# Optimization experiments

Measured on AMD Instinct MI355X. Metric: run time of the kernel, lower is better.

## Reference

```python
import jax, jax.numpy as jnp
import numpy as np

B, N, DIN, D, E, STEP = 4, 1024, 256, 256, 5, 5


def setup_inputs() -> dict:
    key = jax.random.key(0)
    ks = jax.random.split(key, 14)
    s = 0.02  # weight init scale
    inp = {
        "node_features": jax.random.normal(ks[0], (B, N, DIN), dtype=jnp.float32),
        # dense per-edge-type adjacency; scaled so messages stay in a sane range
        "adj_matrices": jax.random.uniform(ks[1], (B, E, N, N), dtype=jnp.float32) * (2.0 / N),
        "fc_in_w": jax.random.normal(ks[2], (D, DIN), dtype=jnp.float32) * s,
        "fc_in_b": jnp.zeros((D,), dtype=jnp.float32),
        "edge_w": jax.random.normal(ks[3], (E, D, D), dtype=jnp.float32) * s,
        "edge_b": jax.random.normal(ks[4], (E, D), dtype=jnp.float32) * s,
        "gru_w_ih": jax.random.normal(ks[5], (3 * D, D), dtype=jnp.float32) * s,
        "gru_w_hh": jax.random.normal(ks[6], (3 * D, D), dtype=jnp.float32) * s,
        "gru_b_ih": jnp.zeros((3 * D,), dtype=jnp.float32),
        "gru_b_hh": jnp.zeros((3 * D,), dtype=jnp.float32),
        "conv1_w": jax.random.normal(ks[7], (D, D), dtype=jnp.float32) * s,
        "conv1_b": jnp.zeros((D,), dtype=jnp.float32),
        "conv2_w": jax.random.normal(ks[8], (D, D), dtype=jnp.float32) * s,
        "conv2_b": jnp.zeros((D,), dtype=jnp.float32),
    }
    return inp


def _gru_cell(x, h, w_ih, w_hh, b_ih, b_hh):
    # torch GRUCell: gates ordered [r, z, n]
    gi = x @ w_ih.T + b_ih  # [B*N, 3D]
    gh = h @ w_hh.T + b_hh
    ir, iz, inn = jnp.split(gi, 3, axis=-1)
    hr, hz, hn = jnp.split(gh, 3, axis=-1)
    r = jax.nn.sigmoid(ir + hr)
    z = jax.nn.sigmoid(iz + hz)
    n = jnp.tanh(inn + r * hn)
    return (1.0 - z) * n + z * h


def reference(node_features, adj_matrices, fc_in_w, fc_in_b, edge_w, edge_b,
              gru_w_ih, gru_w_hh, gru_b_ih, gru_b_hh,
              conv1_w, conv1_b, conv2_w, conv2_b):
    h = node_features @ fc_in_w.T + fc_in_b  # [B, N, D]
    sum_edge_b = jnp.sum(edge_b, axis=0)  # accumulated biases over edge types
    for _ in range(STEP):
        # messages per edge type: adj_e @ h  -> [B, E, N, D]
        msgs = jnp.einsum('benm,bmd->bend', adj_matrices, h)
        # per-edge-type linear (y = x @ W_e.T) then accumulate over edge types
        acc = jnp.einsum('bend,ekd->bnk', msgs, edge_w) + sum_edge_b  # [B, N, D]
        h = _gru_cell(acc, h, gru_w_ih, gru_w_hh, gru_b_ih, gru_b_hh)
    node_states = h  # [B, N, D]
    # conv1d with kernel_size=1 over node axis == per-node linear on channels
    attn_weights = jax.nn.sigmoid(node_states @ conv1_w.T + conv1_b)  # [B, N, D]
    feats = jnp.tanh(node_states @ conv2_w.T + conv2_b)  # [B, N, D]
    graph_embedding = jnp.sum(attn_weights * feats, axis=1)  # sum over nodes -> [B, D]
    attn_map = jnp.mean(attn_weights, axis=2)  # mean over channels -> [B, N]
    return (graph_embedding, node_states, attn_map)
```

## Files before the change

### kernel.cpp

```cpp
#include <hip/hip_runtime.h>
#include <hip/hip_bf16.h>
#include <cstdint>


typedef __attribute__((ext_vector_type(8))) short bf16x8;
typedef __attribute__((ext_vector_type(4))) float f32x4;

__device__ __forceinline__ float bf2f(__hip_bfloat16 x) { return __bfloat162float(x); }
__device__ __forceinline__ __hip_bfloat16 f2bf(float x) { return __float2bfloat16(x); }
__device__ __forceinline__ short f2bs(float x) {
  __hip_bfloat16 h = __float2bfloat16(x);
  return *reinterpret_cast<short*>(&h);
}
__device__ __forceinline__ float s2f(short x) {
  __hip_bfloat16 h = *reinterpret_cast<__hip_bfloat16*>(&x);
  return __bfloat162float(h);
}

__device__ __forceinline__ bf16x8 ld8_ext(const void* base, long off, bool f32) {
  if (f32) {
    const float* p = (const float*)base + off;
    bf16x8 r;
#pragma unroll
    for (int i = 0; i < 8; ++i) r[i] = f2bs(p[i]);
    return r;
  }
  return *(const bf16x8*)((const __hip_bfloat16*)base + off);
}

__device__ __forceinline__ bf16x8 ld8_sum5(const __hip_bfloat16* part, int row, int k) {
  const long base = (long)row * 256 + (long)(row >> 10) * 1048576 + k;
  float s[8] = {0.f, 0.f, 0.f, 0.f, 0.f, 0.f, 0.f, 0.f};
#pragma unroll
  for (int e = 0; e < 5; ++e) {
    bf16x8 v = *(const bf16x8*)(part + base + e * 262144);
#pragma unroll
    for (int j = 0; j < 8; ++j) s[j] += s2f(v[j]);
  }
  bf16x8 r;
#pragma unroll
  for (int j = 0; j < 8; ++j) r[j] = f2bs(s[j]);
  return r;
}

__global__ void detect_dtype(const uint32_t* __restrict__ raw, int* __restrict__ flag) {
  __shared__ int cnt;
  if (threadIdx.x == 0) cnt = 0;
  __syncthreads();
  int c = 0;
  for (int i = threadIdx.x; i < 512; i += 256) {
    uint32_t byte = (raw[i] >> 8) & 0xFF;
    if (byte >= 0x28 && byte <= 0x40) ++c;
  }
  atomicAdd(&cnt, c);
  __syncthreads();
  if (threadIdx.x == 0) *flag = (cnt < 300) ? 1 : 0;
}

__global__ void prep_pool(const void* fcb, const void* bih, const void* bhh,
                          const void* c1b, const void* c2b, const void* edgeb,
                          const int* __restrict__ flag,
                          float* __restrict__ pool, float* __restrict__ ge,
                          float* __restrict__ am32) {
  const bool f32 = (*flag != 0);
  for (int t = threadIdx.x; t < 2560; t += 256) {
    const void* p; int i;
    if (t < 256)       { p = fcb;  i = t; }
    else if (t < 1024) { p = bih;  i = t - 256; }
    else if (t < 1792) { p = bhh;  i = t - 1024; }
    else if (t < 2048) { p = c1b;  i = t - 1792; }
    else if (t < 2304) { p = c2b;  i = t - 2048; }
    else {
      int k = t - 2304; float s = 0.f;
      for (int e = 0; e < 5; ++e)
        s += f32 ? ((const float*)edgeb)[e * 256 + k]
                 : bf2f(((const __hip_bfloat16*)edgeb)[e * 256 + k]);
      pool[t] = s; continue;
    }
    pool[t] = f32 ? ((const float*)p)[i] : bf2f(((const __hip_bfloat16*)p)[i]);
  }
  for (int t = threadIdx.x; t < 1024; t += 256) ge[t] = 0.f;
  for (int t = threadIdx.x; t < 4096; t += 256) am32[t] = 0.f;
}

__global__ void bias_gi_k(const float* __restrict__ pool,
                          const __hip_bfloat16* __restrict__ wih,
                          float* __restrict__ out) {
  const int n = blockIdx.x * 256 + threadIdx.x;
  if (n >= 768) return;
  float s = pool[256 + n];
  for (int k = 0; k < 256; ++k) s += pool[2304 + k] * bf2f(wih[n * 256 + k]);
  out[n] = s;
}

__global__ void wcvt_all(const void* fcw, const void* edw, const void* wih,
                         const void* whh, const void* c1w, const void* c2w,
                         const int* __restrict__ flag, __hip_bfloat16* __restrict__ dst) {
  const bool f32 = (*flag != 0);
  const int i = blockIdx.x * 256 + threadIdx.x;
  const void* src; int off;
  if      (i < 65536)  { src = fcw; off = i; }
  else if (i < 393216) { src = edw; off = i - 65536; }
  else if (i < 589824) { src = wih; off = i - 393216; }
  else if (i < 786432) { src = whh; off = i - 589824; }
  else if (i < 851968) { src = c1w; off = i - 786432; }
  else                 { src = c2w; off = i - 851968; }
  dst[i] = f32 ? f2bf(((const float*)src)[off])
               : ((const __hip_bfloat16*)src)[off];
}

__global__ void adj_cvt(const void* __restrict__ src, const int* __restrict__ flag,
                        __hip_bfloat16* __restrict__ dst) {
  const bool f32 = (*flag != 0);
  const long i = ((long)blockIdx.x * 256 + threadIdx.x) * 8;
  bf16x8 r;
  if (f32) {
    const float* p = (const float*)src + i;
#pragma unroll
    for (int j = 0; j < 8; ++j) r[j] = f2bs(p[j]);
  } else {
    r = *(const bf16x8*)((const __hip_bfloat16*)src + i);
  }
  *(bf16x8*)(dst + i) = r;
}

template<int OUT_MODE, bool HAS_BIAS, int A_MODE, bool DUAL>
__global__ __launch_bounds__(256)
void gemm_bt(const void* __restrict__ A, const __hip_bfloat16* __restrict__ Bt,
             const float* __restrict__ bias, void* __restrict__ Cp,
             const void* __restrict__ A2, const __hip_bfloat16* __restrict__ Bt2,
             const float* __restrict__ bias2, void* __restrict__ Cp2,
             const int* __restrict__ flag,
             int Kg, int ngrp, int lda, int ldb, int ldc,
             long aBatch, int zdivA, int zmodA,
             long bBatch, int zdivB, int zmodB,
             long cBatch, int zdivC, long aGrp, long bGrp, int zSplit)
{
  __shared__ __align__(16) __hip_bfloat16 sA[64 * 64];
  __shared__ __align__(16) __hip_bfloat16 sB[64 * 64];
  const bool af32 = (A_MODE == 1) ? (*flag != 0) : false;
  const int t = threadIdx.x;
  const int w = t >> 6;
  const int l = t & 63;
  const int m0 = blockIdx.x * 64;
  const int n0 = blockIdx.y * 64;
  int z = blockIdx.z;

  const void* Au = A; const __hip_bfloat16* Btu = Bt;
  const float* biasu = bias; void* Cpu = Cp;
  bool second = false;
  if (DUAL && z >= zSplit) {
    Au = A2; Btu = Bt2; biasu = bias2; Cpu = Cp2; z -= zSplit; second = true;
  }

  const long aOff = (long)((z / zdivA) % zmodA) * aBatch;
  const __hip_bfloat16* Bb = Btu + (long)((z / zdivB) % zmodB) * bBatch;

  const int p0 = t, p1 = t + 256;
  const int sr0 = p0 >> 3, sc0 = (p0 & 7) ^ (sr0 & 7);
  const int sr1 = p1 >> 3, sc1 = (p1 & 7) ^ (sr1 & 7);

  f32x4 acc[4];
#pragma unroll
  for (int i = 0; i < 4; ++i) acc[i] = (f32x4){0.f, 0.f, 0.f, 0.f};

  const int mrow = w * 16 + (l & 15);
  const int quad = l >> 4;

  for (int g = 0; g < ngrp; ++g) {
    const long aG = aOff + (long)g * aGrp;
    const __hip_bfloat16* Bg = Bb + (long)g * bGrp;
    for (int k0 = 0; k0 < Kg; k0 += 64) {
      bf16x8 a0, a1;
      if (A_MODE == 2 && !second) {
        a0 = ld8_sum5((const __hip_bfloat16*)Au, m0 + sr0, k0 + sc0 * 8);
        a1 = ld8_sum5((const __hip_bfloat16*)Au, m0 + sr1, k0 + sc1 * 8);
      } else if (A_MODE == 1) {
        a0 = ld8_ext(Au, aG + (long)(m0 + sr0) * lda + (k0 + sc0 * 8), af32);
        a1 = ld8_ext(Au, aG + (long)(m0 + sr1) * lda + (k0 + sc1 * 8), af32);
      } else {
        const __hip_bfloat16* Ab = (const __hip_bfloat16*)Au;
        a0 = *(const bf16x8*)(Ab + aG + (long)(m0 + sr0) * lda + (k0 + sc0 * 8));
        a1 = *(const bf16x8*)(Ab + aG + (long)(m0 + sr1) * lda + (k0 + sc1 * 8));
      }
      bf16x8 b0 = *(const bf16x8*)(Bg + (long)(n0 + sr0) * ldb + (k0 + sc0 * 8));
      bf16x8 b1 = *(const bf16x8*)(Bg + (long)(n0 + sr1) * ldb + (k0 + sc1 * 8));
      __syncthreads();
      *(bf16x8*)(sA + p0 * 8) = a0;
      *(bf16x8*)(sA + p1 * 8) = a1;
      *(bf16x8*)(sB + p0 * 8) = b0;
      *(bf16x8*)(sB + p1 * 8) = b1;
      __syncthreads();
#pragma unroll
      for (int ks = 0; ks < 2; ++ks) {
        const int cg = ks * 4 + quad;
        bf16x8 af = *(const bf16x8*)(sA + mrow * 64 + ((cg ^ (mrow & 7)) * 8));
#pragma unroll
        for (int t4 = 0; t4 < 4; ++t4) {
          const int nrow = t4 * 16 + (l & 15);
          bf16x8 bfr = *(const bf16x8*)(sB + nrow * 64 + ((cg ^ (nrow & 7)) * 8));
          acc[t4] = __builtin_amdgcn_mfma_f32_16x16x32_bf16(af, bfr, acc[t4], 0, 0, 0);
        }
      }
    }
  }

  const long cOff = (long)(z / zdivC) * cBatch;
#pragma unroll
  for (int t4 = 0; t4 < 4; ++t4) {
    const int n = n0 + t4 * 16 + (l & 15);
    float bv = 0.f;
    if (HAS_BIAS) bv = biasu[n];
#pragma unroll
    for (int r = 0; r < 4; ++r) {
      const int m = m0 + w * 16 + quad * 4 + r;
      const float v = acc[t4][r] + bv;
      if (OUT_MODE == 0)
        ((__hip_bfloat16*)Cpu)[cOff + (long)m * ldc + n] = f2bf(v);
      else
        ((float*)Cpu)[cOff + (long)m * ldc + n] = v;
    }
  }
}

__global__ void gru_gate(const __hip_bfloat16* __restrict__ gi,
                         const __hip_bfloat16* __restrict__ gh,
                         __hip_bfloat16* __restrict__ hbf,
                         void* __restrict__ ns_out, const int* __restrict__ flag)
{
  const int m = blockIdx.x;
  const int k = threadIdx.x;
  const long gb = (long)m * 768;
  const float ir = bf2f(gi[gb + k]);
  const float iz = bf2f(gi[gb + 256 + k]);
  const float inn = bf2f(gi[gb + 512 + k]);
  const float hr = bf2f(gh[gb + k]);
  const float hz = bf2f(gh[gb + 256 + k]);
  const float hn = bf2f(gh[gb + 512 + k]);
  const long hidx = (long)m * 256 + k;
  const float h = bf2f(hbf[hidx]);
  const float r = 1.f / (1.f + __expf(-(ir + hr)));
  const float zz = 1.f / (1.f + __expf(-(iz + hz)));
  const float nn = tanhf(inn + r * hn);
  const float hnew = (1.f - zz) * nn + zz * h;
  const __hip_bfloat16 hb = f2bf(hnew);
  hbf[hidx] = hb;
  if (ns_out) {
    if (*flag) ((float*)ns_out)[1024 + hidx] = hnew;
    else       ((__hip_bfloat16*)ns_out)[1024 + hidx] = hb;
  }
}

__global__ __launch_bounds__(256)
void conv_fused(const __hip_bfloat16* __restrict__ hbf,
                const __hip_bfloat16* __restrict__ c1w,
                const __hip_bfloat16* __restrict__ c2w,
                const float* __restrict__ pool,
                float* __restrict__ geg, float* __restrict__ am32)
{
  __shared__ __align__(16) __hip_bfloat16 sA[64 * 64];
  __shared__ __align__(16) __hip_bfloat16 sB1[64 * 64];
  __shared__ __align__(16) __hip_bfloat16 sB2[64 * 64];
  __shared__ float sge[64];
  __shared__ float sam[64];
  const int t = threadIdx.x, w = t >> 6, l = t & 63;
  const int m0 = blockIdx.x * 64, n0 = blockIdx.y * 64;
  if (t < 64) { sge[t] = 0.f; sam[t] = 0.f; }
  const int p0 = t, p1 = t + 256;
  const int sr0 = p0 >> 3, sc0 = (p0 & 7) ^ (sr0 & 7);
  const int sr1 = p1 >> 3, sc1 = (p1 & 7) ^ (sr1 & 7);
  f32x4 a1[4], a2[4];
#pragma unroll
  for (int i = 0; i < 4; ++i) { a1[i] = (f32x4){0,0,0,0}; a2[i] = (f32x4){0,0,0,0}; }
  const int mrow = w * 16 + (l & 15);
  const int quad = l >> 4;
  for (int k0 = 0; k0 < 256; k0 += 64) {
    bf16x8 va0 = *(const bf16x8*)(hbf + (long)(m0 + sr0) * 256 + (k0 + sc0 * 8));
    bf16x8 va1 = *(const bf16x8*)(hbf + (long)(m0 + sr1) * 256 + (k0 + sc1 * 8));
    bf16x8 vb0 = *(const bf16x8*)(c1w + (long)(n0 + sr0) * 256 + (k0 + sc0 * 8));
    bf16x8 vb1 = *(const bf16x8*)(c1w + (long)(n0 + sr1) * 256 + (k0 + sc1 * 8));
    bf16x8 vc0 = *(const bf16x8*)(c2w + (long)(n0 + sr0) * 256 + (k0 + sc0 * 8));
    bf16x8 vc1 = *(const bf16x8*)(c2w + (long)(n0 + sr1) * 256 + (k0 + sc1 * 8));
    __syncthreads();
    *(bf16x8*)(sA + p0 * 8) = va0;  *(bf16x8*)(sA + p1 * 8) = va1;
    *(bf16x8*)(sB1 + p0 * 8) = vb0; *(bf16x8*)(sB1 + p1 * 8) = vb1;
    *(bf16x8*)(sB2 + p0 * 8) = vc0; *(bf16x8*)(sB2 + p1 * 8) = vc1;
    __syncthreads();
#pragma unroll
    for (int ks = 0; ks < 2; ++ks) {
      const int cg = ks * 4 + quad;
      bf16x8 af = *(const bf16x8*)(sA + mrow * 64 + ((cg ^ (mrow & 7)) * 8));
#pragma unroll
      for (int t4 = 0; t4 < 4; ++t4) {
        const int nrow = t4 * 16 + (l & 15);
        bf16x8 b1f = *(const bf16x8*)(sB1 + nrow * 64 + ((cg ^ (nrow & 7)) * 8));
        bf16x8 b2f = *(const bf16x8*)(sB2 + nrow * 64 + ((cg ^ (nrow & 7)) * 8));
        a1[t4] = __builtin_amdgcn_mfma_f32_16x16x32_bf16(af, b1f, a1[t4], 0, 0, 0);
        a2[t4] = __builtin_amdgcn_mfma_f32_16x16x32_bf16(af, b2f, a2[t4], 0, 0, 0);
      }
    }
  }
  float asum[4] = {0.f, 0.f, 0.f, 0.f};
#pragma unroll
  for (int t4 = 0; t4 < 4; ++t4) {
    const int n = n0 + t4 * 16 + (l & 15);
    const float bb1 = pool[1792 + n], bb2 = pool[2048 + n];
    float g = 0.f;
#pragma unroll
    for (int r = 0; r < 4; ++r) {
      const float av = 1.f / (1.f + __expf(-(a1[t4][r] + bb1)));
      const float fv = tanhf(a2[t4][r] + bb2);
      g += av * fv;
      asum[r] += av;
    }
    atomicAdd(&sge[t4 * 16 + (l & 15)], g);
  }
#pragma unroll
  for (int r = 0; r < 4; ++r) atomicAdd(&sam[w * 16 + quad * 4 + r], asum[r]);
  __syncthreads();
  if (t < 64) atomicAdd(&geg[(m0 >> 10) * 256 + n0 + t], sge[t]);
  else if (t < 128) atomicAdd(&am32[m0 + (t - 64)], sam[t - 64]);
}

__global__ void finish_out(const float* __restrict__ ge, const float* __restrict__ am32,
                           void* __restrict__ dout, const int* __restrict__ flag)
{
  const int t = blockIdx.x * 256 + threadIdx.x;
  const bool f32 = (*flag != 0);
  if (t < 1024) {
    if (f32) ((float*)dout)[t] = ge[t];
    else     ((__hip_bfloat16*)dout)[t] = f2bf(ge[t]);
  } else {
    const float v = am32[t - 1024] * (1.f / 256.f);
    if (f32) ((float*)dout)[1049600 + t - 1024] = v;
    else     ((__hip_bfloat16*)dout)[1049600 + t - 1024] = f2bf(v);
  }
}

extern "C" void kernel_launch(void* const* d_in, const int* in_sizes, int n_in,
                              void* d_out, int out_size, void* d_ws, size_t ws_size,
                              hipStream_t stream) {
  (void)in_sizes; (void)n_in; (void)out_size;
  const void* node_f = d_in[0];
  const void* adj    = d_in[1];
  const void* fc_w   = d_in[2];
  const void* fc_b   = d_in[3];
  const void* edge_w = d_in[4];
  const void* edge_b = d_in[5];
  const void* w_ih   = d_in[6];
  const void* w_hh   = d_in[7];
  const void* b_ih   = d_in[8];
  const void* b_hh   = d_in[9];
  const void* c1w    = d_in[10];
  const void* c1b    = d_in[11];
  const void* c2w    = d_in[12];
  const void* c2b    = d_in[13];

  char* ws = (char*)d_ws;
  const size_t MB = (size_t)1 << 20;
  int*            flag = (int*)(ws);
  float*          bp   = (float*)(ws + 256);
  float*          ge   = (float*)(ws + 14336);
  float*          am32 = (float*)(ws + 18432);
  __hip_bfloat16* wbf  = (__hip_bfloat16*)(ws + 34816);
  __hip_bfloat16* hbf  = (__hip_bfloat16*)(ws + 1869824);
  char*           S    = ws + 3966976;
  __hip_bfloat16* heT  = (__hip_bfloat16*)(S);
  __hip_bfloat16* part = (__hip_bfloat16*)(S + 10 * MB);
  __hip_bfloat16* gi   = (__hip_bfloat16*)(S + 20 * MB);
  __hip_bfloat16* gh   = (__hip_bfloat16*)(S + 26 * MB);
  __hip_bfloat16* adjb = (__hip_bfloat16*)(ws + 40 * MB);

  const bool has_split = ws_size >= 38 * MB;
  const bool has_adjb  = ws_size >= 81 * MB;

  detect_dtype<<<1, 256, 0, stream>>>((const uint32_t*)adj, flag);
  prep_pool<<<1, 256, 0, stream>>>(fc_b, b_ih, b_hh, c1b, c2b, edge_b, flag, bp, ge, am32);
  wcvt_all<<<3584, 256, 0, stream>>>(fc_w, edge_w, w_ih, w_hh, c1w, c2w, flag, wbf);
  bias_gi_k<<<3, 256, 0, stream>>>(bp, wbf + 393216, bp + 2560);
  if (has_adjb) adj_cvt<<<10240, 256, 0, stream>>>(adj, flag, adjb);

  gemm_bt<0, true, 1, false><<<dim3(64, 4, 1), 256, 0, stream>>>(
      node_f, wbf + 0, bp + 0, hbf, nullptr, nullptr, nullptr, nullptr, flag,
      256, 1, 256, 256, 256, 0, 1, 1, 0, 1, 1, 0, 1, 0, 0, 0);

  for (int s = 0; s < 5; ++s) {
    gemm_bt<0, false, 0, false><<<dim3(4, 16, 20), 256, 0, stream>>>(
        wbf + 65536, hbf, nullptr, heT, nullptr, nullptr, nullptr, nullptr, flag,
        256, 1, 256, 256, 1024,
        65536, 1, 5, 262144, 5, 4,
        262144, 1, 0, 0, 0);
    if (has_split) {
      if (has_adjb) {
        gemm_bt<0, false, 0, false><<<dim3(16, 4, 20), 256, 0, stream>>>(
            adjb, heT, nullptr, part, nullptr, nullptr, nullptr, nullptr, flag,
            1024, 1, 1024, 1024, 256,
            1048576, 1, 20, 262144, 1, 20,
            262144, 1, 0, 0, 0);
      } else {
        gemm_bt<0, false, 1, false><<<dim3(16, 4, 20), 256, 0, stream>>>(
            adj, heT, nullptr, part, nullptr, nullptr, nullptr, nullptr, flag,
            1024, 1, 1024, 1024, 256,
            1048576, 1, 20, 262144, 1, 20,
            262144, 1, 0, 0, 0);
      }
      gemm_bt<0, true, 2, true><<<dim3(64, 12, 2), 256, 0, stream>>>(
          part, wbf + 393216, bp + 2560, gi,
          hbf,  wbf + 589824, bp + 1024, gh, flag,
          256, 1, 256, 256, 768, 0, 1, 1, 0, 1, 1, 0, 1, 0, 0, 1);
    } else {
      gemm_bt<0, true, 1, false><<<dim3(16, 4, 4), 256, 0, stream>>>(
          adj, heT, bp + 2304, part, nullptr, nullptr, nullptr, nullptr, flag,
          1024, 5, 1024, 1024, 256,
          (long)5 * 1048576, 1, 4, (long)5 * 262144, 1, 4,
          262144, 1, 1048576, 262144, 0);
      gemm_bt<0, true, 0, true><<<dim3(64, 12, 2), 256, 0, stream>>>(
          part, wbf + 393216, bp + 256, gi,
          hbf,  wbf + 589824, bp + 1024, gh, flag,
          256, 1, 256, 256, 768, 0, 1, 1, 0, 1, 1, 0, 1, 0, 0, 1);
    }
    gru_gate<<<4096, 256, 0, stream>>>(gi, gh, hbf,
                                       (s == 4) ? d_out : nullptr, flag);
  }

  conv_fused<<<dim3(64, 4), 256, 0, stream>>>(hbf, wbf + 786432, wbf + 851968,
                                              bp, ge, am32);
  finish_out<<<20, 256, 0, stream>>>(ge, am32, d_out, flag);
}
```

Baseline: 447.6 us.

## Use 128x128 direct-to-LDS MFMA GEMM, pre-summed partials, vectorized GRU gate

```diff
diff --git a/kernel.cpp b/kernel.cpp
--- a/kernel.cpp
+++ b/kernel.cpp
@@ -41,6 +41,12 @@
 #pragma unroll
   for (int j = 0; j < 8; ++j) r[j] = f2bs(s[j]);
   return r;
+}
+
+__device__ __forceinline__ void gload16(const __hip_bfloat16* g, __hip_bfloat16* l) {
+  __builtin_amdgcn_global_load_lds(
+      (const __attribute__((address_space(1))) void*)g,
+      (__attribute__((address_space(3))) void*)l, 16, 0, 0);
 }
 
 __global__ void detect_dtype(const uint32_t* __restrict__ raw, int* __restrict__ flag) {
@@ -122,6 +128,112 @@
     r = *(const bf16x8*)((const __hip_bfloat16*)src + i);
   }
   *(bf16x8*)(dst + i) = r;
+}
+
+__global__ void sum_part(const __hip_bfloat16* __restrict__ part,
+                         __hip_bfloat16* __restrict__ out) {
+  const int t = blockIdx.x * 256 + threadIdx.x;
+  const int row = t >> 5;
+  const int k = (t & 31) * 8;
+  const long base = (long)row * 256 + (long)(row >> 10) * 1048576 + k;
+  float s[8] = {0.f, 0.f, 0.f, 0.f, 0.f, 0.f, 0.f, 0.f};
+#pragma unroll
+  for (int e = 0; e < 5; ++e) {
+    bf16x8 v = *(const bf16x8*)(part + base + e * 262144);
+#pragma unroll
+    for (int j = 0; j < 8; ++j) s[j] += s2f(v[j]);
+  }
+  bf16x8 r;
+#pragma unroll
+  for (int j = 0; j < 8; ++j) r[j] = f2bs(s[j]);
+  *(bf16x8*)(out + (long)row * 256 + k) = r;
+}
+
+template<bool HAS_BIAS, bool DUAL>
+__global__ __launch_bounds__(256)
+void gemm128(const __hip_bfloat16* __restrict__ A, const __hip_bfloat16* __restrict__ Bt,
+             const float* __restrict__ bias, __hip_bfloat16* __restrict__ C,
+             const __hip_bfloat16* __restrict__ A2, const __hip_bfloat16* __restrict__ Bt2,
+             const float* __restrict__ bias2, __hip_bfloat16* __restrict__ C2,
+             int K, int lda, int ldb, int ldc,
+             long aBatch, int zdivA, int zmodA,
+             long bBatch, int zdivB, int zmodB,
+             long cBatch, int zdivC, int zSplit)
+{
+  __shared__ __align__(16) __hip_bfloat16 sA[128 * 64];
+  __shared__ __align__(16) __hip_bfloat16 sB[128 * 64];
+  const int t = threadIdx.x;
+  const int w = t >> 6;
+  const int l = t & 63;
+  const int m0 = blockIdx.x * 128;
+  const int n0 = blockIdx.y * 128;
+  int z = blockIdx.z;
+
+  const __hip_bfloat16* Au = A; const __hip_bfloat16* Btu = Bt;
+  const float* biasu = bias; __hip_bfloat16* Cu = C;
+  if (DUAL && z >= zSplit) { Au = A2; Btu = Bt2; biasu = bias2; Cu = C2; z -= zSplit; }
+
+  const __hip_bfloat16* Ab = Au + (long)((z / zdivA) % zmodA) * aBatch;
+  const __hip_bfloat16* Bb = Btu + (long)((z / zdivB) % zmodB) * bBatch;
+
+  const int srow = l >> 3;
+  const int scol = (l & 7) * 8;
+
+  f32x4 acc[4][4];
+#pragma unroll
+  for (int i = 0; i < 4; ++i)
+#pragma unroll
+    for (int j = 0; j < 4; ++j) acc[i][j] = (f32x4){0.f, 0.f, 0.f, 0.f};
+
+  const int wr = (w >> 1) * 64;
+  const int wc = (w & 1) * 64;
+  const int r15 = l & 15;
+  const int quad = l >> 4;
+
+  for (int k0 = 0; k0 < K; k0 += 64) {
+    __syncthreads();
+#pragma unroll
+    for (int i = 0; i < 4; ++i) {
+      const int c = w * 4 + i;
+      const int row = c * 8 + srow;
+      gload16(Ab + (long)(m0 + row) * lda + (k0 + scol), sA + c * 512);
+      gload16(Bb + (long)(n0 + row) * ldb + (k0 + scol), sB + c * 512);
+    }
+    __syncthreads();
+#pragma unroll
+    for (int ks = 0; ks < 2; ++ks) {
+      const int cg = (ks * 4 + quad) * 8;
+      bf16x8 aF[4], bF[4];
+#pragma unroll
+      for (int i = 0; i < 4; ++i)
+        aF[i] = *(const bf16x8*)(sA + (wr + i * 16 + r15) * 64 + cg);
+#pragma unroll
+      for (int i = 0; i < 4; ++i)
+        bF[i] = *(const bf16x8*)(sB + (wc + i * 16 + r15) * 64 + cg);
+#pragma unroll
+      for (int mi = 0; mi < 4; ++mi)
+#pragma unroll
+        for (int ni = 0; ni < 4; ++ni)
+          acc[mi][ni] = __builtin_amdgcn_mfma_f32_16x16x32_bf16(
+              aF[mi], bF[ni], acc[mi][ni], 0, 0, 0);
+    }
+  }
+
+  const long cOff = (long)(z / zdivC) * cBatch;
+#pragma unroll
+  for (int mi = 0; mi < 4; ++mi) {
+#pragma unroll
+    for (int ni = 0; ni < 4; ++ni) {
+      const int n = n0 + wc + ni * 16 + r15;
+      float bv = 0.f;
+      if (HAS_BIAS) bv = biasu[n];
+#pragma unroll
+      for (int r = 0; r < 4; ++r) {
+        const int m = m0 + wr + mi * 16 + quad * 4 + r;
+        Cu[cOff + (long)m * ldc + n] = f2bf(acc[mi][ni][r] + bv);
+      }
+    }
+  }
 }
 
 template<int OUT_MODE, bool HAS_BIAS, int A_MODE, bool DUAL>
@@ -223,31 +335,42 @@
   }
 }
 
-__global__ void gru_gate(const __hip_bfloat16* __restrict__ gi,
-                         const __hip_bfloat16* __restrict__ gh,
-                         __hip_bfloat16* __restrict__ hbf,
-                         void* __restrict__ ns_out, const int* __restrict__ flag)
+__global__ void gru_gate8(const __hip_bfloat16* __restrict__ gi,
+                          const __hip_bfloat16* __restrict__ gh,
+                          __hip_bfloat16* __restrict__ hbf,
+                          void* __restrict__ ns_out, const int* __restrict__ flag)
 {
-  const int m = blockIdx.x;
-  const int k = threadIdx.x;
-  const long gb = (long)m * 768;
-  const float ir = bf2f(gi[gb + k]);
-  const float iz = bf2f(gi[gb + 256 + k]);
-  const float inn = bf2f(gi[gb + 512 + k]);
-  const float hr = bf2f(gh[gb + k]);
-  const float hz = bf2f(gh[gb + 256 + k]);
-  const float hn = bf2f(gh[gb + 512 + k]);
+  const int t = blockIdx.x * 256 + threadIdx.x;
+  const int m = t >> 5;
+  const int k = (t & 31) * 8;
+  const long gb = (long)m * 768 + k;
+  bf16x8 vir = *(const bf16x8*)(gi + gb);
+  bf16x8 viz = *(const bf16x8*)(gi + gb + 256);
+  bf16x8 vin = *(const bf16x8*)(gi + gb + 512);
+  bf16x8 vhr = *(const bf16x8*)(gh + gb);
+  bf16x8 vhz = *(const bf16x8*)(gh + gb + 256);
+  bf16x8 vhn = *(const bf16x8*)(gh + gb + 512);
   const long hidx = (long)m * 256 + k;
-  const float h = bf2f(hbf[hidx]);
-  const float r = 1.f / (1.f + __expf(-(ir + hr)));
-  const float zz = 1.f / (1.f + __expf(-(iz + hz)));
-  const float nn = tanhf(inn + r * hn);
-  const float hnew = (1.f - zz) * nn + zz * h;
-  const __hip_bfloat16 hb = f2bf(hnew);
-  hbf[hidx] = hb;
+  bf16x8 vh = *(const bf16x8*)(hbf + hidx);
+  bf16x8 out;
+  float hf[8];
+#pragma unroll
+  for (int j = 0; j < 8; ++j) {
+    const float r = 1.f / (1.f + __expf(-(s2f(vir[j]) + s2f(vhr[j]))));
+    const float zz = 1.f / (1.f + __expf(-(s2f(viz[j]) + s2f(vhz[j]))));
+    const float nn = tanhf(s2f(vin[j]) + r * s2f(vhn[j]));
+    hf[j] = (1.f - zz) * nn + zz * s2f(vh[j]);
+    out[j] = f2bs(hf[j]);
+  }
+  *(bf16x8*)(hbf + hidx) = out;
   if (ns_out) {
-    if (*flag) ((float*)ns_out)[1024 + hidx] = hnew;
-    else       ((__hip_bfloat16*)ns_out)[1024 + hidx] = hb;
+    if (*flag) {
+      float* o = (float*)ns_out + 1024 + hidx;
+#pragma unroll
+      for (int j = 0; j < 8; ++j) o[j] = hf[j];
+    } else {
+      *(bf16x8*)((__hip_bfloat16*)ns_out + 1024 + hidx) = out;
+    }
   }
 }
 
@@ -369,6 +492,7 @@
   __hip_bfloat16* part = (__hip_bfloat16*)(S + 10 * MB);
   __hip_bfloat16* gi   = (__hip_bfloat16*)(S + 20 * MB);
   __hip_bfloat16* gh   = (__hip_bfloat16*)(S + 26 * MB);
+  __hip_bfloat16* spt  = (__hip_bfloat16*)(S + 32 * MB);
   __hip_bfloat16* adjb = (__hip_bfloat16*)(ws + 40 * MB);
 
   const bool has_split = ws_size >= 38 * MB;
@@ -385,30 +509,46 @@
       256, 1, 256, 256, 256, 0, 1, 1, 0, 1, 1, 0, 1, 0, 0, 0);
 
   for (int s = 0; s < 5; ++s) {
-    gemm_bt<0, false, 0, false><<<dim3(4, 16, 20), 256, 0, stream>>>(
-        wbf + 65536, hbf, nullptr, heT, nullptr, nullptr, nullptr, nullptr, flag,
-        256, 1, 256, 256, 1024,
-        65536, 1, 5, 262144, 5, 4,
-        262144, 1, 0, 0, 0);
-    if (has_split) {
-      if (has_adjb) {
-        gemm_bt<0, false, 0, false><<<dim3(16, 4, 20), 256, 0, stream>>>(
-            adjb, heT, nullptr, part, nullptr, nullptr, nullptr, nullptr, flag,
-            1024, 1, 1024, 1024, 256,
-            1048576, 1, 20, 262144, 1, 20,
-            262144, 1, 0, 0, 0);
-      } else {
-        gemm_bt<0, false, 1, false><<<dim3(16, 4, 20), 256, 0, stream>>>(
-            adj, heT, nullptr, part, nullptr, nullptr, nullptr, nullptr, flag,
-            1024, 1, 1024, 1024, 256,
-            1048576, 1, 20, 262144, 1, 20,
-            262144, 1, 0, 0, 0);
-      }
+    if (has_adjb) {
+      gemm128<false, false><<<dim3(2, 8, 20), 256, 0, stream>>>(
+          wbf + 65536, hbf, nullptr, heT, nullptr, nullptr, nullptr, nullptr,
+          256, 256, 256, 1024,
+          65536, 1, 5,
+          262144, 5, 4,
+          262144, 1, 0);
+      gemm128<false, false><<<dim3(8, 2, 20), 256, 0, stream>>>(
+          adjb, heT, nullptr, part, nullptr, nullptr, nullptr, nullptr,
+          1024, 1024, 1024, 256,
+          1048576, 1, 20,
+          262144, 1, 20,
+          262144, 1, 0);
+      sum_part<<<512, 256, 0, stream>>>(part, spt);
+      gemm128<true, true><<<dim3(32, 6, 2), 256, 0, stream>>>(
+          spt, wbf + 393216, bp + 2560, gi,
+          hbf, wbf + 589824, bp + 1024, gh,
+          256, 256, 256, 768,
+          0, 1, 1, 0, 1, 1, 0, 1, 1);
+    } else if (has_split) {
+      gemm_bt<0, false, 0, false><<<dim3(4, 16, 20), 256, 0, stream>>>(
+          wbf + 65536, hbf, nullptr, heT, nullptr, nullptr, nullptr, nullptr, flag,
+          256, 1, 256, 256, 1024,
+          65536, 1, 5, 262144, 5, 4,
+          262144, 1, 0, 0, 0);
+      gemm_bt<0, false, 1, false><<<dim3(16, 4, 20), 256, 0, stream>>>(
+          adj, heT, nullptr, part, nullptr, nullptr, nullptr, nullptr, flag,
+          1024, 1, 1024, 1024, 256,
+          1048576, 1, 20, 262144, 1, 20,
+          262144, 1, 0, 0, 0);
       gemm_bt<0, true, 2, true><<<dim3(64, 12, 2), 256, 0, stream>>>(
           part, wbf + 393216, bp + 2560, gi,
           hbf,  wbf + 589824, bp + 1024, gh, flag,
           256, 1, 256, 256, 768, 0, 1, 1, 0, 1, 1, 0, 1, 0, 0, 1);
     } else {
+      gemm_bt<0, false, 0, false><<<dim3(4, 16, 20), 256, 0, stream>>>(
+          wbf + 65536, hbf, nullptr, heT, nullptr, nullptr, nullptr, nullptr, flag,
+          256, 1, 256, 256, 1024,
+          65536, 1, 5, 262144, 5, 4,
+          262144, 1, 0, 0, 0);
       gemm_bt<0, true, 1, false><<<dim3(16, 4, 4), 256, 0, stream>>>(
           adj, heT, bp + 2304, part, nullptr, nullptr, nullptr, nullptr, flag,
           1024, 5, 1024, 1024, 256,
@@ -419,7 +559,7 @@
           hbf,  wbf + 589824, bp + 1024, gh, flag,
           256, 1, 256, 256, 768, 0, 1, 1, 0, 1, 1, 0, 1, 0, 0, 1);
     }
-    gru_gate<<<4096, 256, 0, stream>>>(gi, gh, hbf,
+    gru_gate8<<<512, 256, 0, stream>>>(gi, gh, hbf,
                                        (s == 4) ? d_out : nullptr, flag);
   }
 
```

After: 500.1 us. +11.7%, slower.
